# Kernel tuning notes

Measured on AMD Instinct MI355X. Metric: run time of the kernel, lower is better.

Reference implementation:

```python
import jax, jax.numpy as jnp
import numpy as np

B, N, IN_F, OUT_F = 32, 1024, 256, 256
ALPHA = 0.2  # LeakyReLU negative slope
NEG_INF = -9e15  # matches torch's -9000000000000000.0 masking constant


def setup_inputs() -> dict:
    key = jax.random.key(0)
    k1, k2, k3, k4 = jax.random.split(key, 4)
    h = jax.random.normal(k1, (B, N, IN_F), dtype=jnp.float32)
    adj = jax.random.randint(k2, (B, N, N), 0, 2, dtype=jnp.int32)
    W = jax.random.normal(k3, (OUT_F, IN_F), dtype=jnp.float32) * 0.05
    a = jax.random.normal(k4, (1, 2 * OUT_F), dtype=jnp.float32) * 0.05
    return {"h": h, "adj": adj, "W": W, "a": a}


def reference(h, adj, W, a):
    # Wh: (B, N, out)
    Wh = jnp.einsum("bni,oi->bno", h, W)
    # Decompose a([Wh_i || Wh_j]) = Wh_i . a1 + Wh_j . a2 (identical math,
    # avoids the O(B*N^2*2*out) concat intermediate of the torch code).
    a1 = a[0, :OUT_F]   # (out,)
    a2 = a[0, OUT_F:]   # (out,)
    si = Wh @ a1        # (B, N) score contribution of source node i
    sj = Wh @ a2        # (B, N) score contribution of neighbor node j
    e = jax.nn.leaky_relu(si[:, :, None] + sj[:, None, :], negative_slope=ALPHA)
    attention = jnp.where(adj > 0, e, NEG_INF)
    attention = jax.nn.softmax(attention, axis=-1)
    # dropout omitted (eval mode)
    h_prime = jnp.einsum("bij,bjo->bio", attention, Wh)
    return jax.nn.elu(h_prime)
```

## Files before the change

### kernel.cpp

```cpp
#include <hip/hip_runtime.h>
#include <hip/hip_bf16.h>


#define ALPHA 0.2f

typedef __bf16 bf16x8 __attribute__((ext_vector_type(8)));
typedef __bf16 bf16x4 __attribute__((ext_vector_type(4)));
typedef float  f32x4  __attribute__((ext_vector_type(4)));
typedef unsigned long long u64;

__global__ __launch_bounds__(256) void k0_mask(const int* __restrict__ adj,
                                               u64* __restrict__ mask) {
    const int wid = (blockIdx.x * 256 + threadIdx.x) >> 6;
    const int l   = threadIdx.x & 63;
    const size_t base = (size_t)wid * 64;
    #pragma unroll 4
    for (int it = 0; it < 64; ++it) {
        const size_t word = base + it;
        const int v = adj[word * 64 + l];
        const u64 m = __ballot(v > 0);
        if (l == 0) mask[word] = m;
    }
}

__global__ __launch_bounds__(256) void k1_gemm1(const float* __restrict__ h,
                                                const float* __restrict__ W,
                                                const float* __restrict__ a_g,
                                                __bf16* __restrict__ whT,
                                                float* __restrict__ si,
                                                float* __restrict__ sj) {
    __shared__ __bf16 hA[64 * 72];
    __shared__ __bf16 hB[256 * 72];
    __shared__ float  red[512];
    const int t    = threadIdx.x;
    const int r0   = blockIdx.x * 64;
    const int b    = r0 >> 10;
    const int n0   = r0 & 1023;
    const int w    = t >> 6;
    const int l    = t & 63;
    const int ln   = l & 15;
    const int quad = l >> 4;

    f32x4 acc[4][4] = {};
    float4 ha_r[4], wb_r[16];

    #pragma unroll
    for (int it = 0; it < 4; ++it)
        ha_r[it] = *(const float4*)&h[(size_t)(r0 + it * 16 + (t >> 4)) * 256 + (t & 15) * 4];
    #pragma unroll
    for (int it = 0; it < 16; ++it)
        wb_r[it] = *(const float4*)&W[(size_t)(it * 16 + (t >> 4)) * 256 + (t & 15) * 4];

    for (int kc = 0; kc < 4; ++kc) {
        #pragma unroll
        for (int it = 0; it < 4; ++it) {
            const float4 v = ha_r[it];
            bf16x4 pv = {(__bf16)v.x, (__bf16)v.y, (__bf16)v.z, (__bf16)v.w};
            *(bf16x4*)&hA[(it * 16 + (t >> 4)) * 72 + (t & 15) * 4] = pv;
        }
        #pragma unroll
        for (int it = 0; it < 16; ++it) {
            const float4 v = wb_r[it];
            bf16x4 pv = {(__bf16)v.x, (__bf16)v.y, (__bf16)v.z, (__bf16)v.w};
            *(bf16x4*)&hB[(it * 16 + (t >> 4)) * 72 + (t & 15) * 4] = pv;
        }
        __syncthreads();
        if (kc < 3) {
            const int k0 = (kc + 1) * 64;
            #pragma unroll
            for (int it = 0; it < 4; ++it)
                ha_r[it] = *(const float4*)&h[(size_t)(r0 + it * 16 + (t >> 4)) * 256 + k0 + (t & 15) * 4];
            #pragma unroll
            for (int it = 0; it < 16; ++it)
                wb_r[it] = *(const float4*)&W[(size_t)(it * 16 + (t >> 4)) * 256 + k0 + (t & 15) * 4];
        }
        #pragma unroll
        for (int kk = 0; kk < 2; ++kk) {
            bf16x8 af[4], bfr[4];
            #pragma unroll
            for (int ri = 0; ri < 4; ++ri)
                af[ri] = *(const bf16x8*)&hA[(ri * 16 + ln) * 72 + kk * 32 + quad * 8];
            #pragma unroll
            for (int oi = 0; oi < 4; ++oi)
                bfr[oi] = *(const bf16x8*)&hB[(w * 64 + oi * 16 + ln) * 72 + kk * 32 + quad * 8];
            #pragma unroll
            for (int ri = 0; ri < 4; ++ri)
                #pragma unroll
                for (int oi = 0; oi < 4; ++oi)
                    acc[ri][oi] = __builtin_amdgcn_mfma_f32_16x16x32_bf16(
                        af[ri], bfr[oi], acc[ri][oi], 0, 0, 0);
        }
        __syncthreads();
    }

    #pragma unroll
    for (int ri = 0; ri < 4; ++ri) {
        const int n = ri * 16 + quad * 4;
        #pragma unroll
        for (int oi = 0; oi < 4; ++oi) {
            const int o = w * 64 + oi * 16 + ln;
            bf16x4 pv = {(__bf16)acc[ri][oi][0], (__bf16)acc[ri][oi][1],
                         (__bf16)acc[ri][oi][2], (__bf16)acc[ri][oi][3]};
            *(bf16x4*)&hB[o * 72 + n] = pv;
        }
    }
    __syncthreads();

    #pragma unroll
    for (int it = 0; it < 8; ++it) {
        const int o   = w * 64 + it * 8 + (l >> 3);
        const int seg = l & 7;
        const bf16x8 v = *(const bf16x8*)&hB[o * 72 + seg * 8];
        *(bf16x8*)&whT[((size_t)b * 256 + o) * 1024 + n0 + seg * 8] = v;
    }

    {
        float s1 = 0.f, s2 = 0.f;
        #pragma unroll 8
        for (int oi = 0; oi < 64; ++oi) {
            const int o = w * 64 + oi;
            const float v = (float)hB[o * 72 + l];
            s1 += v * a_g[o];
            s2 += v * a_g[256 + o];
        }
        red[w * 64 + l]       = s1;
        red[256 + w * 64 + l] = s2;
    }
    __syncthreads();
    if (t < 64) {
        si[b * 1024 + n0 + t] = red[t] + red[64 + t] + red[128 + t] + red[192 + t];
    } else if (t < 128) {
        const int n = t - 64;
        sj[b * 1024 + n0 + n] = red[256 + n] + red[320 + n] + red[384 + n] + red[448 + n];
    }
}

__global__ __launch_bounds__(256) void k3_attn(const u64* __restrict__ mask,
                                               const __bf16* __restrict__ whT,
                                               const float* __restrict__ si_g,
                                               const float* __restrict__ sj_g,
                                               float* __restrict__ out) {
    __shared__ __bf16 lds_w[256 * 72];
    __shared__ __bf16 lds_s[64 * 72];
    __shared__ float  lds_denom[64];
    const int t    = threadIdx.x;
    const int b    = blockIdx.y;
    const int i0   = blockIdx.x * 64;
    const int w    = t >> 6;
    const int l    = t & 63;
    const int ln   = l & 15;
    const int quad = l >> 4;
    const int g    = t >> 4;
    const int j4   = t & 15;

    float si_r[4];
    #pragma unroll
    for (int m = 0; m < 4; ++m) si_r[m] = si_g[b * 1024 + i0 + m * 16 + g];

    float dsum[4] = {0.f, 0.f, 0.f, 0.f};
    f32x4 acc[4][4] = {};
    const __bf16* whTb  = whT + (size_t)b * 256 * 1024;
    const u64*    maskb = mask + ((size_t)b * 1024) * 16;

    bf16x8 vreg[8];
    u64    msk[4];
    float4 sjv;

    #pragma unroll
    for (int it = 0; it < 8; ++it)
        vreg[it] = *(const bf16x8*)&whTb[(size_t)(it * 32 + (t >> 3)) * 1024 + (t & 7) * 8];
    #pragma unroll
    for (int m = 0; m < 4; ++m) msk[m] = maskb[(size_t)(i0 + m * 16 + g) * 16];
    sjv = *(const float4*)&sj_g[b * 1024 + j4 * 4];

    for (int jc = 0; jc < 16; ++jc) {
        const int j0 = jc * 64;
        #pragma unroll
        for (int it = 0; it < 8; ++it)
            *(bf16x8*)&lds_w[(it * 32 + (t >> 3)) * 72 + (t & 7) * 8] = vreg[it];
        #pragma unroll
        for (int m = 0; m < 4; ++m) {
            const int il   = m * 16 + g;
            const unsigned bits = (unsigned)(msk[m] >> (4 * j4)) & 0xFu;
            float e0 = si_r[m] + sjv.x; e0 = e0 > 0.f ? e0 : ALPHA * e0;
            float e1 = si_r[m] + sjv.y; e1 = e1 > 0.f ? e1 : ALPHA * e1;
            float e2 = si_r[m] + sjv.z; e2 = e2 > 0.f ? e2 : ALPHA * e2;
            float e3 = si_r[m] + sjv.w; e3 = e3 > 0.f ? e3 : ALPHA * e3;
            const float w0 = (bits & 1u) ? __expf(e0) : 0.f;
            const float w1 = (bits & 2u) ? __expf(e1) : 0.f;
            const float w2 = (bits & 4u) ? __expf(e2) : 0.f;
            const float w3 = (bits & 8u) ? __expf(e3) : 0.f;
            bf16x4 pv = {(__bf16)w0, (__bf16)w1, (__bf16)w2, (__bf16)w3};
            dsum[m] += (float)pv[0] + (float)pv[1] + (float)pv[2] + (float)pv[3];
            *(bf16x4*)&lds_s[il * 72 + j4 * 4] = pv;
        }
        __syncthreads();
        if (jc < 15) {
            const int j1 = j0 + 64;
            #pragma unroll
            for (int it = 0; it < 8; ++it)
                vreg[it] = *(const bf16x8*)&whTb[(size_t)(it * 32 + (t >> 3)) * 1024 + j1 + (t & 7) * 8];
            #pragma unroll
            for (int m = 0; m < 4; ++m)
                msk[m] = maskb[(size_t)(i0 + m * 16 + g) * 16 + jc + 1];
            sjv = *(const float4*)&sj_g[b * 1024 + j1 + j4 * 4];
        }
        #pragma unroll
        for (int kk = 0; kk < 2; ++kk) {
            bf16x8 af[4], bfr[4];
            #pragma unroll
            for (int ri = 0; ri < 4; ++ri)
                af[ri] = *(const bf16x8*)&lds_s[(ri * 16 + ln) * 72 + kk * 32 + quad * 8];
            #pragma unroll
            for (int oi = 0; oi < 4; ++oi)
                bfr[oi] = *(const bf16x8*)&lds_w[(w * 64 + oi * 16 + ln) * 72 + kk * 32 + quad * 8];
            #pragma unroll
            for (int ri = 0; ri < 4; ++ri)
                #pragma unroll
                for (int oi = 0; oi < 4; ++oi)
                    acc[ri][oi] = __builtin_amdgcn_mfma_f32_16x16x32_bf16(
                        af[ri], bfr[oi], acc[ri][oi], 0, 0, 0);
        }
        __syncthreads();
    }

    #pragma unroll
    for (int m = 0; m < 4; ++m) {
        float v = dsum[m];
        v += __shfl_xor(v, 1);
        v += __shfl_xor(v, 2);
        v += __shfl_xor(v, 4);
        v += __shfl_xor(v, 8);
        if (j4 == 0) lds_denom[m * 16 + g] = v;
    }
    __syncthreads();
    #pragma unroll
    for (int ri = 0; ri < 4; ++ri) {
        #pragma unroll
        for (int q = 0; q < 4; ++q) {
            const int il = ri * 16 + quad * 4 + q;
            const float dinv = 1.0f / fmaxf(lds_denom[il], 1e-30f);
            #pragma unroll
            for (int oi = 0; oi < 4; ++oi) {
                const int o = w * 64 + oi * 16 + ln;
                const float v = acc[ri][oi][q] * dinv;
                const float r = v > 0.f ? v : __expf(v) - 1.f;
                out[((size_t)(b * 1024 + i0 + il)) * 256 + o] = r;
            }
        }
    }
}

extern "C" void kernel_launch(void* const* d_in, const int* in_sizes, int n_in,
                              void* d_out, int out_size, void* d_ws, size_t ws_size,
                              hipStream_t stream) {
    const float* h   = (const float*)d_in[0];
    const int*   adj = (const int*)d_in[1];
    const float* W   = (const float*)d_in[2];
    const float* a   = (const float*)d_in[3];
    float* out = (float*)d_out;

    __bf16* whT  = (__bf16*)d_ws;
    float*  si   = (float*)((char*)d_ws + (size_t)16777216);
    float*  sj   = (float*)((char*)d_ws + (size_t)16777216 + 131072);
    u64*    mask = (u64*)((char*)d_ws + (size_t)16777216 + 262144);

    k0_mask<<<2048, 256, 0, stream>>>(adj, mask);
    k1_gemm1<<<512, 256, 0, stream>>>(h, W, a, whT, si, sj);
    k3_attn<<<dim3(16, 32), 256, 0, stream>>>(mask, whT, si, sj, out);
}
```

Before: 286.3 us.

## Fuse mask and projection kernels; halve attention row tile and read Wh directly

The adjacency-bitmask kernel and the Wh projection GEMM are merged into one launch: blocks at index 512 and above build the mask, the rest do the GEMM. This removes one kernel launch and lets the two independent jobs overlap. The attention kernel now handles 32 query rows per block instead of 64, which doubles the grid. It also loads the Wh^T MFMA operands straight from global memory into registers, dropping the LDS staging buffer and the next-chunk register prefetch. LDS use and register pressure fall, so occupancy should rise, but each Wh tile is re-read by twice as many blocks and global load latency is no longer hidden by explicit prefetch.

```diff
diff --git a/kernel.cpp b/kernel.cpp
--- a/kernel.cpp
+++ b/kernel.cpp
@@ -9,30 +9,33 @@
 typedef float  f32x4  __attribute__((ext_vector_type(4)));
 typedef unsigned long long u64;
 
-__global__ __launch_bounds__(256) void k0_mask(const int* __restrict__ adj,
-                                               u64* __restrict__ mask) {
-    const int wid = (blockIdx.x * 256 + threadIdx.x) >> 6;
-    const int l   = threadIdx.x & 63;
-    const size_t base = (size_t)wid * 64;
-    #pragma unroll 4
-    for (int it = 0; it < 64; ++it) {
-        const size_t word = base + it;
-        const int v = adj[word * 64 + l];
-        const u64 m = __ballot(v > 0);
-        if (l == 0) mask[word] = m;
-    }
-}
-
-__global__ __launch_bounds__(256) void k1_gemm1(const float* __restrict__ h,
-                                                const float* __restrict__ W,
-                                                const float* __restrict__ a_g,
-                                                __bf16* __restrict__ whT,
-                                                float* __restrict__ si,
-                                                float* __restrict__ sj) {
+__global__ __launch_bounds__(256) void k01_fused(const float* __restrict__ h,
+                                                 const float* __restrict__ W,
+                                                 const float* __restrict__ a_g,
+                                                 const int* __restrict__ adj,
+                                                 __bf16* __restrict__ whT,
+                                                 float* __restrict__ si,
+                                                 float* __restrict__ sj,
+                                                 u64* __restrict__ mask) {
     __shared__ __bf16 hA[64 * 72];
     __shared__ __bf16 hB[256 * 72];
     __shared__ float  red[512];
-    const int t    = threadIdx.x;
+    const int t = threadIdx.x;
+
+    if (blockIdx.x >= 512) {
+        const int wid = ((blockIdx.x - 512) * 256 + t) >> 6;
+        const int l   = t & 63;
+        const size_t base = (size_t)wid * 64;
+        #pragma unroll 4
+        for (int it = 0; it < 64; ++it) {
+            const size_t word = base + it;
+            const int v = adj[word * 64 + l];
+            const u64 m = __ballot(v > 0);
+            if (l == 0) mask[word] = m;
+        }
+        return;
+    }
+
     const int r0   = blockIdx.x * 64;
     const int b    = r0 >> 10;
     const int n0   = r0 & 1023;
@@ -140,12 +143,11 @@
                                                const float* __restrict__ si_g,
                                                const float* __restrict__ sj_g,
                                                float* __restrict__ out) {
-    __shared__ __bf16 lds_w[256 * 72];
-    __shared__ __bf16 lds_s[64 * 72];
-    __shared__ float  lds_denom[64];
+    __shared__ __bf16 lds_s[32 * 72];
+    __shared__ float  lds_denom[32];
     const int t    = threadIdx.x;
     const int b    = blockIdx.y;
-    const int i0   = blockIdx.x * 64;
+    const int i0   = blockIdx.x * 32;
     const int w    = t >> 6;
     const int l    = t & 63;
     const int ln   = l & 15;
@@ -153,34 +155,32 @@
     const int g    = t >> 4;
     const int j4   = t & 15;
 
-    float si_r[4];
-    #pragma unroll
-    for (int m = 0; m < 4; ++m) si_r[m] = si_g[b * 1024 + i0 + m * 16 + g];
-
-    float dsum[4] = {0.f, 0.f, 0.f, 0.f};
-    f32x4 acc[4][4] = {};
+    float si_r[2];
+    #pragma unroll
+    for (int m = 0; m < 2; ++m) si_r[m] = si_g[b * 1024 + i0 + m * 16 + g];
+
+    float dsum[2] = {0.f, 0.f};
+    f32x4 acc[2][4] = {};
     const __bf16* whTb  = whT + (size_t)b * 256 * 1024;
     const u64*    maskb = mask + ((size_t)b * 1024) * 16;
 
-    bf16x8 vreg[8];
-    u64    msk[4];
-    float4 sjv;
-
-    #pragma unroll
-    for (int it = 0; it < 8; ++it)
-        vreg[it] = *(const bf16x8*)&whTb[(size_t)(it * 32 + (t >> 3)) * 1024 + (t & 7) * 8];
-    #pragma unroll
-    for (int m = 0; m < 4; ++m) msk[m] = maskb[(size_t)(i0 + m * 16 + g) * 16];
-    sjv = *(const float4*)&sj_g[b * 1024 + j4 * 4];
-
     for (int jc = 0; jc < 16; ++jc) {
         const int j0 = jc * 64;
-        #pragma unroll
-        for (int it = 0; it < 8; ++it)
-            *(bf16x8*)&lds_w[(it * 32 + (t >> 3)) * 72 + (t & 7) * 8] = vreg[it];
-        #pragma unroll
-        for (int m = 0; m < 4; ++m) {
-            const int il   = m * 16 + g;
+        bf16x8 bfr[2][4];
+        #pragma unroll
+        for (int kk = 0; kk < 2; ++kk)
+            #pragma unroll
+            for (int oi = 0; oi < 4; ++oi)
+                bfr[kk][oi] = *(const bf16x8*)&whTb[(size_t)(w * 64 + oi * 16 + ln) * 1024
+                                                    + j0 + kk * 32 + quad * 8];
+        u64 msk[2];
+        #pragma unroll
+        for (int m = 0; m < 2; ++m) msk[m] = maskb[(size_t)(i0 + m * 16 + g) * 16 + jc];
+        const float4 sjv = *(const float4*)&sj_g[b * 1024 + j0 + j4 * 4];
+
+        #pragma unroll
+        for (int m = 0; m < 2; ++m) {
+            const int il = m * 16 + g;
             const unsigned bits = (unsigned)(msk[m] >> (4 * j4)) & 0xFu;
             float e0 = si_r[m] + sjv.x; e0 = e0 > 0.f ? e0 : ALPHA * e0;
             float e1 = si_r[m] + sjv.y; e1 = e1 > 0.f ? e1 : ALPHA * e1;
@@ -195,37 +195,24 @@
             *(bf16x4*)&lds_s[il * 72 + j4 * 4] = pv;
         }
         __syncthreads();
-        if (jc < 15) {
-            const int j1 = j0 + 64;
-            #pragma unroll
-            for (int it = 0; it < 8; ++it)
-                vreg[it] = *(const bf16x8*)&whTb[(size_t)(it * 32 + (t >> 3)) * 1024 + j1 + (t & 7) * 8];
-            #pragma unroll
-            for (int m = 0; m < 4; ++m)
-                msk[m] = maskb[(size_t)(i0 + m * 16 + g) * 16 + jc + 1];
-            sjv = *(const float4*)&sj_g[b * 1024 + j1 + j4 * 4];
-        }
         #pragma unroll
         for (int kk = 0; kk < 2; ++kk) {
-            bf16x8 af[4], bfr[4];
-            #pragma unroll
-            for (int ri = 0; ri < 4; ++ri)
+            bf16x8 af[2];
+            #pragma unroll
+            for (int ri = 0; ri < 2; ++ri)
                 af[ri] = *(const bf16x8*)&lds_s[(ri * 16 + ln) * 72 + kk * 32 + quad * 8];
             #pragma unroll
-            for (int oi = 0; oi < 4; ++oi)
-                bfr[oi] = *(const bf16x8*)&lds_w[(w * 64 + oi * 16 + ln) * 72 + kk * 32 + quad * 8];
-            #pragma unroll
-            for (int ri = 0; ri < 4; ++ri)
+            for (int ri = 0; ri < 2; ++ri)
                 #pragma unroll
                 for (int oi = 0; oi < 4; ++oi)
                     acc[ri][oi] = __builtin_amdgcn_mfma_f32_16x16x32_bf16(
-                        af[ri], bfr[oi], acc[ri][oi], 0, 0, 0);
-        }
-        __syncthreads();
-    }
-
-    #pragma unroll
-    for (int m = 0; m < 4; ++m) {
+                        af[ri], bfr[kk][oi], acc[ri][oi], 0, 0, 0);
+        }
+        __syncthreads();
+    }
+
+    #pragma unroll
+    for (int m = 0; m < 2; ++m) {
         float v = dsum[m];
         v += __shfl_xor(v, 1);
         v += __shfl_xor(v, 2);
@@ -235,7 +222,7 @@
     }
     __syncthreads();
     #pragma unroll
-    for (int ri = 0; ri < 4; ++ri) {
+    for (int ri = 0; ri < 2; ++ri) {
         #pragma unroll
         for (int q = 0; q < 4; ++q) {
             const int il = ri * 16 + quad * 4 + q;
@@ -265,7 +252,6 @@
     float*  sj   = (float*)((char*)d_ws + (size_t)16777216 + 131072);
     u64*    mask = (u64*)((char*)d_ws + (size_t)16777216 + 262144);
 
-    k0_mask<<<2048, 256, 0, stream>>>(adj, mask);
-    k1_gemm1<<<512, 256, 0, stream>>>(h, W, a, whT, si, sj);
-    k3_attn<<<dim3(16, 32), 256, 0, stream>>>(mask, whT, si, sj, out);
+    k01_fused<<<2560, 256, 0, stream>>>(h, W, a, adj, whT, si, sj, mask);
+    k3_attn<<<dim3(32, 32), 256, 0, stream>>>(mask, whT, si, sj, out);
 }
```

After: 410.3 us. 1.43x slower.

## Pre-swizzle Wh into MFMA fragment layout and drop LDS staging in attention

Applied to the files above, without the earlier changes.

The projection kernel now writes Wh directly in the per-lane MFMA B-fragment order instead of a transposed row layout. The attention kernel then loads B fragments straight from global memory into registers, with no LDS staging and no barriers. Each wave builds its own attention fragment in registers, covering 16 rows and all 256 outputs, and reduces the softmax denominator with cross-lane shuffles. This removes LDS traffic and synchronisation, but each wave re-reads the whole Wh tile from global or L2 memory, giving four times the redundant reads per block, and raises register pressure to 16 accumulators plus 16 B fragments.

```diff
diff --git a/kernel.cpp b/kernel.cpp
--- a/kernel.cpp
+++ b/kernel.cpp
@@ -26,7 +26,7 @@
 __global__ __launch_bounds__(256) void k1_gemm1(const float* __restrict__ h,
                                                 const float* __restrict__ W,
                                                 const float* __restrict__ a_g,
-                                                __bf16* __restrict__ whT,
+                                                __bf16* __restrict__ whF,
                                                 float* __restrict__ si,
                                                 float* __restrict__ sj) {
     __shared__ __bf16 hA[64 * 72];
@@ -36,6 +36,7 @@
     const int r0   = blockIdx.x * 64;
     const int b    = r0 >> 10;
     const int n0   = r0 & 1023;
+    const int jc   = blockIdx.x & 15;
     const int w    = t >> 6;
     const int l    = t & 63;
     const int ln   = l & 15;
@@ -107,11 +108,11 @@
     __syncthreads();
 
     #pragma unroll
-    for (int it = 0; it < 8; ++it) {
-        const int o   = w * 64 + it * 8 + (l >> 3);
-        const int seg = l & 7;
-        const bf16x8 v = *(const bf16x8*)&hB[o * 72 + seg * 8];
-        *(bf16x8*)&whT[((size_t)b * 256 + o) * 1024 + n0 + seg * 8] = v;
+    for (int fi = 0; fi < 8; ++fi) {
+        const int oi = w * 4 + (fi >> 1);
+        const int kk = fi & 1;
+        const bf16x8 v = *(const bf16x8*)&hB[(oi * 16 + ln) * 72 + kk * 32 + quad * 8];
+        *(bf16x8*)&whF[(size_t)(((b * 16 + jc) * 32) + oi * 2 + kk) * 512 + l * 8] = v;
     }
 
     {
@@ -136,13 +137,10 @@
 }
 
 __global__ __launch_bounds__(256) void k3_attn(const u64* __restrict__ mask,
-                                               const __bf16* __restrict__ whT,
+                                               const __bf16* __restrict__ whF,
                                                const float* __restrict__ si_g,
                                                const float* __restrict__ sj_g,
                                                float* __restrict__ out) {
-    __shared__ __bf16 lds_w[256 * 72];
-    __shared__ __bf16 lds_s[64 * 72];
-    __shared__ float  lds_denom[64];
     const int t    = threadIdx.x;
     const int b    = blockIdx.y;
     const int i0   = blockIdx.x * 64;
@@ -150,103 +148,66 @@
     const int l    = t & 63;
     const int ln   = l & 15;
     const int quad = l >> 4;
-    const int g    = t >> 4;
-    const int j4   = t & 15;
-
-    float si_r[4];
-    #pragma unroll
-    for (int m = 0; m < 4; ++m) si_r[m] = si_g[b * 1024 + i0 + m * 16 + g];
-
-    float dsum[4] = {0.f, 0.f, 0.f, 0.f};
-    f32x4 acc[4][4] = {};
-    const __bf16* whTb  = whT + (size_t)b * 256 * 1024;
-    const u64*    maskb = mask + ((size_t)b * 1024) * 16;
-
-    bf16x8 vreg[8];
-    u64    msk[4];
-    float4 sjv;
-
-    #pragma unroll
-    for (int it = 0; it < 8; ++it)
-        vreg[it] = *(const bf16x8*)&whTb[(size_t)(it * 32 + (t >> 3)) * 1024 + (t & 7) * 8];
-    #pragma unroll
-    for (int m = 0; m < 4; ++m) msk[m] = maskb[(size_t)(i0 + m * 16 + g) * 16];
-    sjv = *(const float4*)&sj_g[b * 1024 + j4 * 4];
+
+    const int irow = i0 + w * 16 + ln;
+    const float si_r = si_g[b * 1024 + irow];
+    const u64* mrow  = mask + (size_t)(b * 1024 + irow) * 16;
+    const __bf16* whFb = whF + (size_t)b * 16 * 16384;
+    const float* sjb = sj_g + b * 1024;
+
+    f32x4 acc[16] = {};
+    float dsum = 0.f;
 
     for (int jc = 0; jc < 16; ++jc) {
-        const int j0 = jc * 64;
-        #pragma unroll
-        for (int it = 0; it < 8; ++it)
-            *(bf16x8*)&lds_w[(it * 32 + (t >> 3)) * 72 + (t & 7) * 8] = vreg[it];
-        #pragma unroll
-        for (int m = 0; m < 4; ++m) {
-            const int il   = m * 16 + g;
-            const unsigned bits = (unsigned)(msk[m] >> (4 * j4)) & 0xFu;
-            float e0 = si_r[m] + sjv.x; e0 = e0 > 0.f ? e0 : ALPHA * e0;
-            float e1 = si_r[m] + sjv.y; e1 = e1 > 0.f ? e1 : ALPHA * e1;
-            float e2 = si_r[m] + sjv.z; e2 = e2 > 0.f ? e2 : ALPHA * e2;
-            float e3 = si_r[m] + sjv.w; e3 = e3 > 0.f ? e3 : ALPHA * e3;
-            const float w0 = (bits & 1u) ? __expf(e0) : 0.f;
-            const float w1 = (bits & 2u) ? __expf(e1) : 0.f;
-            const float w2 = (bits & 4u) ? __expf(e2) : 0.f;
-            const float w3 = (bits & 8u) ? __expf(e3) : 0.f;
-            bf16x4 pv = {(__bf16)w0, (__bf16)w1, (__bf16)w2, (__bf16)w3};
-            dsum[m] += (float)pv[0] + (float)pv[1] + (float)pv[2] + (float)pv[3];
-            *(bf16x4*)&lds_s[il * 72 + j4 * 4] = pv;
-        }
-        __syncthreads();
-        if (jc < 15) {
-            const int j1 = j0 + 64;
-            #pragma unroll
-            for (int it = 0; it < 8; ++it)
-                vreg[it] = *(const bf16x8*)&whTb[(size_t)(it * 32 + (t >> 3)) * 1024 + j1 + (t & 7) * 8];
-            #pragma unroll
-            for (int m = 0; m < 4; ++m)
-                msk[m] = maskb[(size_t)(i0 + m * 16 + g) * 16 + jc + 1];
-            sjv = *(const float4*)&sj_g[b * 1024 + j1 + j4 * 4];
-        }
+        const u64 m64 = mrow[jc];
         #pragma unroll
         for (int kk = 0; kk < 2; ++kk) {
-            bf16x8 af[4], bfr[4];
-            #pragma unroll
-            for (int ri = 0; ri < 4; ++ri)
-                af[ri] = *(const bf16x8*)&lds_s[(ri * 16 + ln) * 72 + kk * 32 + quad * 8];
-            #pragma unroll
-            for (int oi = 0; oi < 4; ++oi)
-                bfr[oi] = *(const bf16x8*)&lds_w[(w * 64 + oi * 16 + ln) * 72 + kk * 32 + quad * 8];
-            #pragma unroll
-            for (int ri = 0; ri < 4; ++ri)
-                #pragma unroll
-                for (int oi = 0; oi < 4; ++oi)
-                    acc[ri][oi] = __builtin_amdgcn_mfma_f32_16x16x32_bf16(
-                        af[ri], bfr[oi], acc[ri][oi], 0, 0, 0);
-        }
-        __syncthreads();
-    }
-
-    #pragma unroll
-    for (int m = 0; m < 4; ++m) {
-        float v = dsum[m];
-        v += __shfl_xor(v, 1);
-        v += __shfl_xor(v, 2);
-        v += __shfl_xor(v, 4);
-        v += __shfl_xor(v, 8);
-        if (j4 == 0) lds_denom[m * 16 + g] = v;
-    }
-    __syncthreads();
-    #pragma unroll
-    for (int ri = 0; ri < 4; ++ri) {
-        #pragma unroll
-        for (int q = 0; q < 4; ++q) {
-            const int il = ri * 16 + quad * 4 + q;
-            const float dinv = 1.0f / fmaxf(lds_denom[il], 1e-30f);
-            #pragma unroll
-            for (int oi = 0; oi < 4; ++oi) {
-                const int o = w * 64 + oi * 16 + ln;
-                const float v = acc[ri][oi][q] * dinv;
-                const float r = v > 0.f ? v : __expf(v) - 1.f;
-                out[((size_t)(b * 1024 + i0 + il)) * 256 + o] = r;
-            }
+            bf16x8 barr[16];
+            const __bf16* fp = whFb + (size_t)(jc * 32 + kk) * 512 + l * 8;
+            #pragma unroll
+            for (int oi = 0; oi < 16; ++oi)
+                barr[oi] = *(const bf16x8*)(fp + (size_t)oi * 1024);
+            const unsigned bits = (unsigned)(m64 >> (kk * 32 + quad * 8)) & 0xFFu;
+            const float4 s0 = *(const float4*)&sjb[jc * 64 + kk * 32 + quad * 8];
+            const float4 s1 = *(const float4*)&sjb[jc * 64 + kk * 32 + quad * 8 + 4];
+            float e0 = si_r + s0.x; e0 = e0 > 0.f ? e0 : ALPHA * e0;
+            float e1 = si_r + s0.y; e1 = e1 > 0.f ? e1 : ALPHA * e1;
+            float e2 = si_r + s0.z; e2 = e2 > 0.f ? e2 : ALPHA * e2;
+            float e3 = si_r + s0.w; e3 = e3 > 0.f ? e3 : ALPHA * e3;
+            float e4 = si_r + s1.x; e4 = e4 > 0.f ? e4 : ALPHA * e4;
+            float e5 = si_r + s1.y; e5 = e5 > 0.f ? e5 : ALPHA * e5;
+            float e6 = si_r + s1.z; e6 = e6 > 0.f ? e6 : ALPHA * e6;
+            float e7 = si_r + s1.w; e7 = e7 > 0.f ? e7 : ALPHA * e7;
+            bf16x8 af;
+            af[0] = (__bf16)((bits &   1u) ? __expf(e0) : 0.f);
+            af[1] = (__bf16)((bits &   2u) ? __expf(e1) : 0.f);
+            af[2] = (__bf16)((bits &   4u) ? __expf(e2) : 0.f);
+            af[3] = (__bf16)((bits &   8u) ? __expf(e3) : 0.f);
+            af[4] = (__bf16)((bits &  16u) ? __expf(e4) : 0.f);
+            af[5] = (__bf16)((bits &  32u) ? __expf(e5) : 0.f);
+            af[6] = (__bf16)((bits &  64u) ? __expf(e6) : 0.f);
+            af[7] = (__bf16)((bits & 128u) ? __expf(e7) : 0.f);
+            dsum += (float)af[0] + (float)af[1] + (float)af[2] + (float)af[3]
+                  + (float)af[4] + (float)af[5] + (float)af[6] + (float)af[7];
+            #pragma unroll
+            for (int oi = 0; oi < 16; ++oi)
+                acc[oi] = __builtin_amdgcn_mfma_f32_16x16x32_bf16(af, barr[oi], acc[oi], 0, 0, 0);
+        }
+    }
+
+    float tot = dsum;
+    tot += __shfl_xor(tot, 16);
+    tot += __shfl_xor(tot, 32);
+
+    #pragma unroll
+    for (int q = 0; q < 4; ++q) {
+        const float d = __shfl(tot, quad * 4 + q);
+        const float dinv = 1.0f / fmaxf(d, 1e-30f);
+        const size_t rbase = (size_t)(b * 1024 + i0 + w * 16 + quad * 4 + q) * 256;
+        #pragma unroll
+        for (int oi = 0; oi < 16; ++oi) {
+            const float v = acc[oi][q] * dinv;
+            out[rbase + oi * 16 + ln] = v > 0.f ? v : __expf(v) - 1.f;
         }
     }
 }
@@ -260,12 +221,12 @@
     const float* a   = (const float*)d_in[3];
     float* out = (float*)d_out;
 
-    __bf16* whT  = (__bf16*)d_ws;
+    __bf16* whF  = (__bf16*)d_ws;
     float*  si   = (float*)((char*)d_ws + (size_t)16777216);
     float*  sj   = (float*)((char*)d_ws + (size_t)16777216 + 131072);
     u64*    mask = (u64*)((char*)d_ws + (size_t)16777216 + 262144);
 
     k0_mask<<<2048, 256, 0, stream>>>(adj, mask);
-    k1_gemm1<<<512, 256, 0, stream>>>(h, W, a, whT, si, sj);
-    k3_attn<<<dim3(16, 32), 256, 0, stream>>>(mask, whT, si, sj, out);
-}
+    k1_gemm1<<<512, 256, 0, stream>>>(h, W, a, whF, si, sj);
+    k3_attn<<<dim3(16, 32), 256, 0, stream>>>(mask, whF, si, sj, out);
+}
```

Measured after the change: 299.5 us. 1.05x slower.
